# Performance work log

Measured on AMD Instinct MI355X. Metric: run time of the kernel, lower is better.

## Reference

```python
import jax, jax.numpy as jnp
import numpy as np

TOP_K = 2


def setup_inputs() -> dict:
    key = jax.random.key(0)
    k_x, k_g, k_w1, k_w2, k_w3 = jax.random.split(key, 5)
    B, S, D, H, E = 2, 512, 1024, 512, 8
    x = jax.random.normal(k_x, (B, S, D), dtype=jnp.float32)
    gate_w = jax.random.normal(k_g, (D, E), dtype=jnp.float32) * (D ** -0.5)
    w1 = jax.random.normal(k_w1, (E, D, H), dtype=jnp.float32) * 0.02  # gate proj
    w2 = jax.random.normal(k_w2, (E, H, D), dtype=jnp.float32) * 0.02  # down proj
    w3 = jax.random.normal(k_w3, (E, D, H), dtype=jnp.float32) * 0.02  # up proj
    return {"x": x, "gate_w": gate_w, "w1": w1, "w2": w2, "w3": w3}


def reference(x, gate_w, w1, w2, w3):
    # Token-choice top-k MoE with grouped SwiGLU experts, no shared expert.
    # Equivalent to torchtune MoE: gather routed tokens, scale by top-k router
    # score, run per-expert FFN, scatter-add back. Since each expert's FFN has
    # no bias (FFN(0) == 0), the dispatch/grouped-GEMM/combine is expressed
    # densely as sum_e FFN_e(scale[:, e] * x), which is mathematically identical.
    B, S, D = x.shape
    E = gate_w.shape[1]
    xf = x.reshape(B * S, D)                      # [T, D]
    T = B * S

    logits = xf @ gate_w                          # [T, E]
    scores = jax.nn.softmax(logits, axis=-1)
    top_scores, top_idx = jax.lax.top_k(scores, TOP_K)  # [T, k]

    # scale[t, e] = router score if expert e selected for token t, else 0
    scale = jnp.zeros((T, E), dtype=x.dtype).at[
        jnp.arange(T)[:, None], top_idx
    ].set(top_scores)

    xs = scale.T[:, :, None] * xf[None, :, :]     # [E, T, D] scaled routed input
    h = jax.nn.silu(jnp.einsum('etd,edh->eth', xs, w1)) \
        * jnp.einsum('etd,edh->eth', xs, w3)      # [E, T, H]
    y = jnp.einsum('eth,ehd->etd', h, w2)         # [E, T, D]
    out = y.sum(axis=0)                           # combine (scatter-add equiv)
    return out.reshape(B, S, D)
```

## Files before the change

kernel.cpp:

```cpp
#include <hip/hip_runtime.h>
#include <hip/hip_bf16.h>
#include <cstddef>

#define T_TOK 1024
#define D_DIM 1024
#define H_DIM 512
#define E_EXP 8
#define P_CAP 2560
#define MAX_MT (P_CAP / 64)
#define LDA 72

typedef __attribute__((ext_vector_type(4))) float    float4_t;
typedef __attribute__((ext_vector_type(8))) short    short8_t;
typedef __attribute__((ext_vector_type(4))) unsigned uint4_t;

__device__ __forceinline__ short f2bf(float f) {
  union { float f; unsigned u; } v; v.f = f;
  unsigned u = v.u;
  u += 0x7FFFu + ((u >> 16) & 1u);
  return (short)(u >> 16);
}

__device__ __forceinline__ unsigned pkbf(float a, float b) {
  union { __hip_bfloat162 h; unsigned u; } v;
  v.h = __float22bfloat162_rn(make_float2(a, b));
  return v.u;
}

__global__ __launch_bounds__(256) void prep_kernel(
    const float* __restrict__ w1, const float* __restrict__ w3,
    const float* __restrict__ w2, const float* __restrict__ x,
    const float* __restrict__ gw, short* __restrict__ w13t,
    short* __restrict__ w2t, int* __restrict__ idx2,
    float* __restrict__ scale2, float* __restrict__ out) {
  __shared__ float tile[64][68];
  const int z = blockIdx.z;
  const int tid = threadIdx.x;

  if (z < 24) {
    const float* src; short* dst; int N, ldd, row_off;
    if (z < 16) {
      if (blockIdx.y >= 8) return;
      int which = z >> 3, e = z & 7;
      src = (which ? w3 : w1) + (size_t)e * D_DIM * H_DIM;
      dst = w13t + (size_t)e * D_DIM * (2 * H_DIM);
      N = H_DIM; ldd = D_DIM; row_off = which ? H_DIM : 0;
    } else {
      if (blockIdx.x >= 8) return;
      int e = z - 16;
      src = w2 + (size_t)e * H_DIM * D_DIM;
      dst = w2t + (size_t)e * D_DIM * H_DIM;
      N = D_DIM; ldd = H_DIM; row_off = 0;
    }
    const int k0 = blockIdx.x * 64, n0 = blockIdx.y * 64;
    const int kr = tid >> 4, nc = (tid & 15) * 4;
    #pragma unroll
    for (int p = 0; p < 4; ++p) {
      int k = p * 16 + kr;
      float4_t v = *(const float4_t*)(src + (size_t)(k0 + k) * N + n0 + nc);
      *(float4_t*)&tile[k][nc] = v;
    }
    __syncthreads();
    const int r8 = tid >> 3, c8 = tid & 7;
    #pragma unroll
    for (int p = 0; p < 2; ++p) {
      int row = p * 32 + r8;
      uint4_t u;
      #pragma unroll
      for (int j = 0; j < 4; ++j)
        u[j] = pkbf(tile[c8 * 8 + 2 * j][row], tile[c8 * 8 + 2 * j + 1][row]);
      *(uint4_t*)(dst + (size_t)(row_off + n0 + row) * ldd + k0 + c8 * 8) = u;
    }
    return;
  }

  if (z == 25) {
    float4_t z4 = {0.f, 0.f, 0.f, 0.f};
    float4_t* o = (float4_t*)(out + ((size_t)(blockIdx.y * 16 + blockIdx.x)) * 4096);
    #pragma unroll
    for (int i = 0; i < 4; ++i) o[i * 256 + tid] = z4;
    return;
  }

  const int wid  = tid >> 6;
  const int lane = tid & 63;
  const int t = (blockIdx.y * 16 + blockIdx.x) * 4 + wid;
  const float* xr = x + (size_t)t * D_DIM;
  float acc[E_EXP];
  #pragma unroll
  for (int e = 0; e < E_EXP; ++e) acc[e] = 0.f;
  for (int d = lane; d < D_DIM; d += 64) {
    float xv = xr[d];
    float4_t g0 = *(const float4_t*)(gw + d * E_EXP);
    float4_t g1 = *(const float4_t*)(gw + d * E_EXP + 4);
    acc[0] += xv * g0[0]; acc[1] += xv * g0[1];
    acc[2] += xv * g0[2]; acc[3] += xv * g0[3];
    acc[4] += xv * g1[0]; acc[5] += xv * g1[1];
    acc[6] += xv * g1[2]; acc[7] += xv * g1[3];
  }
  #pragma unroll
  for (int off = 32; off >= 1; off >>= 1) {
    #pragma unroll
    for (int e = 0; e < E_EXP; ++e) acc[e] += __shfl_down(acc[e], off, 64);
  }
  if (lane == 0) {
    float m = acc[0];
    #pragma unroll
    for (int e = 1; e < E_EXP; ++e) m = fmaxf(m, acc[e]);
    float p[E_EXP]; float s = 0.f;
    #pragma unroll
    for (int e = 0; e < E_EXP; ++e) { p[e] = __expf(acc[e] - m); s += p[e]; }
    float inv = 1.f / s;
    #pragma unroll
    for (int e = 0; e < E_EXP; ++e) p[e] *= inv;
    int i1 = 0;
    #pragma unroll
    for (int e = 1; e < E_EXP; ++e) if (p[e] > p[i1]) i1 = e;
    int i2 = (i1 == 0) ? 1 : 0;
    #pragma unroll
    for (int e = 0; e < E_EXP; ++e) {
      if (e == i1 || e == i2) continue;
      if (p[e] > p[i2]) i2 = e;
    }
    idx2[2 * t]     = i1;  scale2[2 * t]     = p[i1];
    idx2[2 * t + 1] = i2;  scale2[2 * t + 1] = p[i2];
  }
}

__global__ __launch_bounds__(256) void scan_kernel(
    const int* __restrict__ idx2, const float* __restrict__ scale2,
    int* __restrict__ pair_tok, float* __restrict__ pair_scale,
    int* __restrict__ meta) {
  __shared__ int cnt[E_EXP], base[E_EXP], cur[E_EXP];
  const int tid = threadIdx.x;
  if (tid < E_EXP) { cnt[tid] = 0; cur[tid] = 0; }
  for (int p = tid; p < P_CAP; p += 256) { pair_tok[p] = -1; pair_scale[p] = 0.f; }
  __syncthreads();
  for (int t = tid; t < T_TOK; t += 256) {
    atomicAdd(&cnt[idx2[2 * t]], 1);
    atomicAdd(&cnt[idx2[2 * t + 1]], 1);
  }
  __syncthreads();
  if (tid == 0) {
    int b = 0, g = 0;
    for (int e = 0; e < E_EXP; ++e) {
      base[e] = b;
      int al = (cnt[e] + 63) & ~63;
      for (int j = 0; j < al; j += 64) { meta[1 + g] = e; meta[41 + g] = b + j; ++g; }
      b += al;
    }
    meta[0] = g;
  }
  __syncthreads();
  for (int t = tid; t < T_TOK; t += 256) {
    #pragma unroll
    for (int s = 0; s < 2; ++s) {
      int e = idx2[2 * t + s];
      int p = base[e] + atomicAdd(&cur[e], 1);
      pair_tok[p] = t;
      pair_scale[p] = scale2[2 * t + s];
    }
  }
}

__global__ __launch_bounds__(256, 4) void gemm1_kernel(
    const float* __restrict__ x, const short* __restrict__ w13t,
    const int* __restrict__ pair_tok, const float* __restrict__ pair_scale,
    const int* __restrict__ meta, short* __restrict__ h) {
  __shared__ short As[64 * LDA];
  __shared__ short B1s[32 * LDA];
  __shared__ short B3s[32 * LDA];
  const int mt = blockIdx.y;
  if (mt >= meta[0]) return;
  const int e    = meta[1 + mt];
  const int row0 = meta[41 + mt];
  const int n0   = blockIdx.x * 32;
  const int tid = threadIdx.x, lane = tid & 63, wid = tid >> 6;
  const int wr = wid >> 1, wc = wid & 1;
  const int q = lane >> 4, ln = lane & 15;
  const short* bsrc = w13t + (size_t)e * D_DIM * (2 * H_DIM);

  const int ar = tid >> 2, ak = (tid & 3) * 16;
  const int   tokr = pair_tok[row0 + ar];
  const float sc   = pair_scale[row0 + ar];
  const float* xrow = x + (size_t)(tokr < 0 ? 0 : tokr) * D_DIM + ak;
  const int br = tid >> 3, bu = (tid & 7) * 8;
  const short* b1p = bsrc + (size_t)(n0 + br) * D_DIM + bu;
  const short* b3p = bsrc + (size_t)(H_DIM + n0 + br) * D_DIM + bu;

  float4_t acc1[2], acc3[2];
  acc1[0] = acc1[1] = acc3[0] = acc3[1] = (float4_t){0.f, 0.f, 0.f, 0.f};

  for (int k0 = 0; k0 < D_DIM; k0 += 64) {
    float4_t v0 = *(const float4_t*)(xrow + k0);
    float4_t v1 = *(const float4_t*)(xrow + k0 + 4);
    float4_t v2 = *(const float4_t*)(xrow + k0 + 8);
    float4_t v3 = *(const float4_t*)(xrow + k0 + 12);
    uint4_t vb1 = *(const uint4_t*)(b1p + k0);
    uint4_t vb3 = *(const uint4_t*)(b3p + k0);
    uint4_t u0 = {pkbf(v0[0] * sc, v0[1] * sc), pkbf(v0[2] * sc, v0[3] * sc),
                  pkbf(v1[0] * sc, v1[1] * sc), pkbf(v1[2] * sc, v1[3] * sc)};
    uint4_t u1 = {pkbf(v2[0] * sc, v2[1] * sc), pkbf(v2[2] * sc, v2[3] * sc),
                  pkbf(v3[0] * sc, v3[1] * sc), pkbf(v3[2] * sc, v3[3] * sc)};
    *(uint4_t*)&As[ar * LDA + ak]     = u0;
    *(uint4_t*)&As[ar * LDA + ak + 8] = u1;
    *(uint4_t*)&B1s[br * LDA + bu] = vb1;
    *(uint4_t*)&B3s[br * LDA + bu] = vb3;
    __syncthreads();

    short8_t af[2][2], b1f[2], b3f[2];
    #pragma unroll
    for (int i = 0; i < 2; ++i)
      #pragma unroll
      for (int kk = 0; kk < 2; ++kk)
        af[i][kk] = *(const short8_t*)&As[(wr * 32 + i * 16 + ln) * LDA + kk * 32 + q * 8];
    #pragma unroll
    for (int kk = 0; kk < 2; ++kk) {
      b1f[kk] = *(const short8_t*)&B1s[(wc * 16 + ln) * LDA + kk * 32 + q * 8];
      b3f[kk] = *(const short8_t*)&B3s[(wc * 16 + ln) * LDA + kk * 32 + q * 8];
    }
    #pragma unroll
    for (int i = 0; i < 2; ++i)
      #pragma unroll
      for (int kk = 0; kk < 2; ++kk) {
        acc1[i] = __builtin_amdgcn_mfma_f32_16x16x32_bf16(af[i][kk], b1f[kk], acc1[i], 0, 0, 0);
        acc3[i] = __builtin_amdgcn_mfma_f32_16x16x32_bf16(af[i][kk], b3f[kk], acc3[i], 0, 0, 0);
      }
    __syncthreads();
  }

  #pragma unroll
  for (int i = 0; i < 2; ++i) {
    int r_base = row0 + wr * 32 + i * 16 + q * 4;
    int col = n0 + wc * 16 + ln;
    #pragma unroll
    for (int rr = 0; rr < 4; ++rr) {
      float c1 = acc1[i][rr];
      float c3 = acc3[i][rr];
      float sig = 1.f / (1.f + __expf(-c1));
      h[(size_t)(r_base + rr) * H_DIM + col] = f2bf(c1 * sig * c3);
    }
  }
}

__global__ __launch_bounds__(256, 4) void gemm2_kernel(
    const short* __restrict__ h, const short* __restrict__ w2t,
    const int* __restrict__ pair_tok, const int* __restrict__ meta,
    float* __restrict__ out) {
  __shared__ short As[64 * LDA];
  __shared__ short Bs[64 * LDA];
  const int mt = blockIdx.y;
  if (mt >= meta[0]) return;
  const int e    = meta[1 + mt];
  const int row0 = meta[41 + mt];
  const int n0   = blockIdx.x * 64;
  const int tid = threadIdx.x, lane = tid & 63, wid = tid >> 6;
  const int wr = wid >> 1, wc = wid & 1;
  const int q = lane >> 4, ln = lane & 15;
  const short* bsrc = w2t + (size_t)e * D_DIM * H_DIM;

  const int ar = tid >> 2, ak = (tid & 3) * 16;
  const short* arow = h + (size_t)(row0 + ar) * H_DIM + ak;
  const short* brow = bsrc + (size_t)(n0 + ar) * H_DIM + ak;

  float4_t acc[2][2];
  #pragma unroll
  for (int i = 0; i < 2; ++i)
    #pragma unroll
    for (int j = 0; j < 2; ++j) acc[i][j] = (float4_t){0.f, 0.f, 0.f, 0.f};

  for (int k0 = 0; k0 < H_DIM; k0 += 64) {
    uint4_t va0 = *(const uint4_t*)(arow + k0);
    uint4_t va1 = *(const uint4_t*)(arow + k0 + 8);
    uint4_t vb0 = *(const uint4_t*)(brow + k0);
    uint4_t vb1 = *(const uint4_t*)(brow + k0 + 8);
    *(uint4_t*)&As[ar * LDA + ak]     = va0;
    *(uint4_t*)&As[ar * LDA + ak + 8] = va1;
    *(uint4_t*)&Bs[ar * LDA + ak]     = vb0;
    *(uint4_t*)&Bs[ar * LDA + ak + 8] = vb1;
    __syncthreads();

    short8_t af[2][2], bf[2][2];
    #pragma unroll
    for (int i = 0; i < 2; ++i)
      #pragma unroll
      for (int kk = 0; kk < 2; ++kk) {
        af[i][kk] = *(const short8_t*)&As[(wr * 32 + i * 16 + ln) * LDA + kk * 32 + q * 8];
        bf[i][kk] = *(const short8_t*)&Bs[(wc * 32 + i * 16 + ln) * LDA + kk * 32 + q * 8];
      }
    #pragma unroll
    for (int i = 0; i < 2; ++i)
      #pragma unroll
      for (int j = 0; j < 2; ++j)
        #pragma unroll
        for (int kk = 0; kk < 2; ++kk)
          acc[i][j] = __builtin_amdgcn_mfma_f32_16x16x32_bf16(af[i][kk], bf[j][kk], acc[i][j], 0, 0, 0);
    __syncthreads();
  }

  #pragma unroll
  for (int i = 0; i < 2; ++i) {
    int r_base = row0 + wr * 32 + i * 16 + q * 4;
    #pragma unroll
    for (int rr = 0; rr < 4; ++rr) {
      int tok = pair_tok[r_base + rr];
      if (tok < 0) continue;
      float* orow = out + (size_t)tok * D_DIM;
      #pragma unroll
      for (int j = 0; j < 2; ++j) {
        int col = n0 + wc * 32 + j * 16 + ln;
        atomicAdd(orow + col, acc[i][j][rr]);
      }
    }
  }
}

extern "C" void kernel_launch(void* const* d_in, const int* in_sizes, int n_in,
                              void* d_out, int out_size, void* d_ws, size_t ws_size,
                              hipStream_t stream) {
  const float* x  = (const float*)d_in[0];
  const float* gw = (const float*)d_in[1];
  const float* w1 = (const float*)d_in[2];
  const float* w2 = (const float*)d_in[3];
  const float* w3 = (const float*)d_in[4];
  float* out = (float*)d_out;

  char* ws = (char*)d_ws;
  int*   idx2    = (int*)  (ws);
  float* scale2  = (float*)(ws + 8192);
  int*   ptok    = (int*)  (ws + 16384);
  float* pscale  = (float*)(ws + 32768);
  int*   meta    = (int*)  (ws + 49152);
  short* h       = (short*)(ws + (1u << 20));
  short* w13t    = (short*)(ws + (4u << 20));
  short* w2t     = (short*)(ws + (21u << 20));

  prep_kernel<<<dim3(16, 16, 26), dim3(256), 0, stream>>>(
      w1, w3, w2, x, gw, w13t, w2t, idx2, scale2, out);
  scan_kernel<<<dim3(1), dim3(256), 0, stream>>>(idx2, scale2, ptok, pscale, meta);
  gemm1_kernel<<<dim3(H_DIM / 32, MAX_MT), dim3(256), 0, stream>>>(
      x, w13t, ptok, pscale, meta, h);
  gemm2_kernel<<<dim3(D_DIM / 64, MAX_MT), dim3(256), 0, stream>>>(
      h, w2t, ptok, meta, out);
}
```

Measured before the change: 150.7 us.

## Fuse all four MoE stages into one cooperative persistent kernel with grid syncs

Replaces the four separate launches (prep, scan, gemm1, gemm2) with one cooperative kernel. A persistent grid loops over jobs for each phase, and grid.sync() separates the phases. The goal is to remove launch gaps and the idle tail of grids sized for the worst case, since the GEMM loops now run only over the real number of M-tiles. The cost is grid-wide barriers, a scan phase where only block 0 works while the rest of the grid waits, and lower occupancy from launch_bounds(256,2) and the shared smem buffer.

Measured after the change: 416.8 us. +176.5%, slower.

```diff
diff --git a/kernel.cpp b/kernel.cpp
--- a/kernel.cpp
+++ b/kernel.cpp
@@ -1,13 +1,15 @@
 #include <hip/hip_runtime.h>
+#include <hip/hip_cooperative_groups.h>
 #include <hip/hip_bf16.h>
 #include <cstddef>
+
+namespace cg = cooperative_groups;
 
 #define T_TOK 1024
 #define D_DIM 1024
 #define H_DIM 512
 #define E_EXP 8
 #define P_CAP 2560
-#define MAX_MT (P_CAP / 64)
 #define LDA 72
 
 typedef __attribute__((ext_vector_type(4))) float    float4_t;
@@ -27,289 +29,282 @@
   return v.u;
 }
 
-__global__ __launch_bounds__(256) void prep_kernel(
+__global__ __launch_bounds__(256, 2) void fused_kernel(
     const float* __restrict__ w1, const float* __restrict__ w3,
     const float* __restrict__ w2, const float* __restrict__ x,
     const float* __restrict__ gw, short* __restrict__ w13t,
     short* __restrict__ w2t, int* __restrict__ idx2,
-    float* __restrict__ scale2, float* __restrict__ out) {
-  __shared__ float tile[64][68];
-  const int z = blockIdx.z;
+    float* __restrict__ scale2, int* __restrict__ pair_tok,
+    float* __restrict__ pair_scale, int* __restrict__ meta,
+    short* __restrict__ h, float* __restrict__ out) {
+  cg::grid_group grid = cg::this_grid();
+  __shared__ __align__(16) char smem[18432];
+  const int bid = blockIdx.x;
+  const int nb  = gridDim.x;
   const int tid = threadIdx.x;
-
-  if (z < 24) {
-    const float* src; short* dst; int N, ldd, row_off;
-    if (z < 16) {
-      if (blockIdx.y >= 8) return;
-      int which = z >> 3, e = z & 7;
-      src = (which ? w3 : w1) + (size_t)e * D_DIM * H_DIM;
-      dst = w13t + (size_t)e * D_DIM * (2 * H_DIM);
-      N = H_DIM; ldd = D_DIM; row_off = which ? H_DIM : 0;
+  const int lane = tid & 63, wid = tid >> 6;
+
+  for (int j = bid; j < 3584; j += nb) {
+    if (j < 3072) {
+      float (*tile)[68] = (float(*)[68])smem;
+      int z = j >> 7, sub = j & 127;
+      const float* src; short* dst; int N, ldd, row_off, xt, yt;
+      if (z < 16) {
+        int which = z >> 3, e = z & 7;
+        src = (which ? w3 : w1) + (size_t)e * D_DIM * H_DIM;
+        dst = w13t + (size_t)e * D_DIM * (2 * H_DIM);
+        N = H_DIM; ldd = D_DIM; row_off = which ? H_DIM : 0;
+        xt = sub >> 3; yt = sub & 7;
+      } else {
+        int e = z - 16;
+        src = w2 + (size_t)e * H_DIM * D_DIM;
+        dst = w2t + (size_t)e * D_DIM * H_DIM;
+        N = D_DIM; ldd = H_DIM; row_off = 0;
+        xt = sub & 7; yt = sub >> 3;
+      }
+      const int k0 = xt * 64, n0 = yt * 64;
+      const int kr = tid >> 4, nc = (tid & 15) * 4;
+      #pragma unroll
+      for (int p = 0; p < 4; ++p) {
+        int k = p * 16 + kr;
+        float4_t v = *(const float4_t*)(src + (size_t)(k0 + k) * N + n0 + nc);
+        *(float4_t*)&tile[k][nc] = v;
+      }
+      __syncthreads();
+      const int r8 = tid >> 3, c8 = tid & 7;
+      #pragma unroll
+      for (int p = 0; p < 2; ++p) {
+        int row = p * 32 + r8;
+        uint4_t u;
+        #pragma unroll
+        for (int jj = 0; jj < 4; ++jj)
+          u[jj] = pkbf(tile[c8 * 8 + 2 * jj][row], tile[c8 * 8 + 2 * jj + 1][row]);
+        *(uint4_t*)(dst + (size_t)(row_off + n0 + row) * ldd + k0 + c8 * 8) = u;
+      }
+      __syncthreads();
+    } else if (j < 3328) {
+      const int t = (j - 3072) * 4 + wid;
+      const float* xr = x + (size_t)t * D_DIM;
+      float acc[E_EXP];
+      #pragma unroll
+      for (int e = 0; e < E_EXP; ++e) acc[e] = 0.f;
+      for (int d = lane; d < D_DIM; d += 64) {
+        float xv = xr[d];
+        float4_t g0 = *(const float4_t*)(gw + d * E_EXP);
+        float4_t g1 = *(const float4_t*)(gw + d * E_EXP + 4);
+        acc[0] += xv * g0[0]; acc[1] += xv * g0[1];
+        acc[2] += xv * g0[2]; acc[3] += xv * g0[3];
+        acc[4] += xv * g1[0]; acc[5] += xv * g1[1];
+        acc[6] += xv * g1[2]; acc[7] += xv * g1[3];
+      }
+      #pragma unroll
+      for (int off = 32; off >= 1; off >>= 1) {
+        #pragma unroll
+        for (int e = 0; e < E_EXP; ++e) acc[e] += __shfl_down(acc[e], off, 64);
+      }
+      if (lane == 0) {
+        float m = acc[0];
+        #pragma unroll
+        for (int e = 1; e < E_EXP; ++e) m = fmaxf(m, acc[e]);
+        float p[E_EXP]; float s = 0.f;
+        #pragma unroll
+        for (int e = 0; e < E_EXP; ++e) { p[e] = __expf(acc[e] - m); s += p[e]; }
+        float inv = 1.f / s;
+        #pragma unroll
+        for (int e = 0; e < E_EXP; ++e) p[e] *= inv;
+        int i1 = 0;
+        #pragma unroll
+        for (int e = 1; e < E_EXP; ++e) if (p[e] > p[i1]) i1 = e;
+        int i2 = (i1 == 0) ? 1 : 0;
+        #pragma unroll
+        for (int e = 0; e < E_EXP; ++e) {
+          if (e == i1 || e == i2) continue;
+          if (p[e] > p[i2]) i2 = e;
+        }
+        idx2[2 * t]     = i1;  scale2[2 * t]     = p[i1];
+        idx2[2 * t + 1] = i2;  scale2[2 * t + 1] = p[i2];
+      }
     } else {
-      if (blockIdx.x >= 8) return;
-      int e = z - 16;
-      src = w2 + (size_t)e * H_DIM * D_DIM;
-      dst = w2t + (size_t)e * D_DIM * H_DIM;
-      N = D_DIM; ldd = H_DIM; row_off = 0;
-    }
-    const int k0 = blockIdx.x * 64, n0 = blockIdx.y * 64;
-    const int kr = tid >> 4, nc = (tid & 15) * 4;
+      float4_t z4 = {0.f, 0.f, 0.f, 0.f};
+      float4_t* o = (float4_t*)(out + (size_t)(j - 3328) * 4096);
+      #pragma unroll
+      for (int i = 0; i < 4; ++i) o[i * 256 + tid] = z4;
+    }
+  }
+  grid.sync();
+
+  if (bid == 0) {
+    __shared__ int cnt[E_EXP], base[E_EXP], cur[E_EXP];
+    if (tid < E_EXP) { cnt[tid] = 0; cur[tid] = 0; }
+    for (int p = tid; p < P_CAP; p += 256) { pair_tok[p] = -1; pair_scale[p] = 0.f; }
+    __syncthreads();
+    for (int t = tid; t < T_TOK; t += 256) {
+      atomicAdd(&cnt[idx2[2 * t]], 1);
+      atomicAdd(&cnt[idx2[2 * t + 1]], 1);
+    }
+    __syncthreads();
+    if (tid == 0) {
+      int b = 0, g = 0;
+      for (int e = 0; e < E_EXP; ++e) {
+        base[e] = b;
+        int al = (cnt[e] + 63) & ~63;
+        for (int jj = 0; jj < al; jj += 64) { meta[1 + g] = e; meta[41 + g] = b + jj; ++g; }
+        b += al;
+      }
+      meta[0] = g;
+    }
+    __syncthreads();
+    for (int t = tid; t < T_TOK; t += 256) {
+      #pragma unroll
+      for (int s = 0; s < 2; ++s) {
+        int e = idx2[2 * t + s];
+        int p = base[e] + atomicAdd(&cur[e], 1);
+        pair_tok[p] = t;
+        pair_scale[p] = scale2[2 * t + s];
+      }
+    }
+  }
+  grid.sync();
+
+  const int n_mt = meta[0];
+  const int wr = (tid >> 6) >> 1, wc = (tid >> 6) & 1;
+  const int q = lane >> 4, ln = lane & 15;
+
+  for (int job = bid; job < 16 * n_mt; job += nb) {
+    short* As  = (short*)smem;
+    short* B1s = As + 64 * LDA;
+    short* B3s = B1s + 32 * LDA;
+    const int mt   = job >> 4;
+    const int e    = meta[1 + mt];
+    const int row0 = meta[41 + mt];
+    const int n0   = (job & 15) * 32;
+    const short* bsrc = w13t + (size_t)e * D_DIM * (2 * H_DIM);
+
+    const int ar = tid >> 2, ak = (tid & 3) * 16;
+    const int   tokr = pair_tok[row0 + ar];
+    const float sc   = pair_scale[row0 + ar];
+    const float* xrow = x + (size_t)(tokr < 0 ? 0 : tokr) * D_DIM + ak;
+    const int br = tid >> 3, bu = (tid & 7) * 8;
+    const short* b1p = bsrc + (size_t)(n0 + br) * D_DIM + bu;
+    const short* b3p = bsrc + (size_t)(H_DIM + n0 + br) * D_DIM + bu;
+
+    float4_t acc1[2], acc3[2];
+    acc1[0] = acc1[1] = acc3[0] = acc3[1] = (float4_t){0.f, 0.f, 0.f, 0.f};
+
+    for (int k0 = 0; k0 < D_DIM; k0 += 64) {
+      float4_t v0 = *(const float4_t*)(xrow + k0);
+      float4_t v1 = *(const float4_t*)(xrow + k0 + 4);
+      float4_t v2 = *(const float4_t*)(xrow + k0 + 8);
+      float4_t v3 = *(const float4_t*)(xrow + k0 + 12);
+      uint4_t vb1 = *(const uint4_t*)(b1p + k0);
+      uint4_t vb3 = *(const uint4_t*)(b3p + k0);
+      uint4_t u0 = {pkbf(v0[0] * sc, v0[1] * sc), pkbf(v0[2] * sc, v0[3] * sc),
+                    pkbf(v1[0] * sc, v1[1] * sc), pkbf(v1[2] * sc, v1[3] * sc)};
+      uint4_t u1 = {pkbf(v2[0] * sc, v2[1] * sc), pkbf(v2[2] * sc, v2[3] * sc),
+                    pkbf(v3[0] * sc, v3[1] * sc), pkbf(v3[2] * sc, v3[3] * sc)};
+      *(uint4_t*)&As[ar * LDA + ak]     = u0;
+      *(uint4_t*)&As[ar * LDA + ak + 8] = u1;
+      *(uint4_t*)&B1s[br * LDA + bu] = vb1;
+      *(uint4_t*)&B3s[br * LDA + bu] = vb3;
+      __syncthreads();
+
+      short8_t af[2][2], b1f[2], b3f[2];
+      #pragma unroll
+      for (int i = 0; i < 2; ++i)
+        #pragma unroll
+        for (int kk = 0; kk < 2; ++kk)
+          af[i][kk] = *(const short8_t*)&As[(wr * 32 + i * 16 + ln) * LDA + kk * 32 + q * 8];
+      #pragma unroll
+      for (int kk = 0; kk < 2; ++kk) {
+        b1f[kk] = *(const short8_t*)&B1s[(wc * 16 + ln) * LDA + kk * 32 + q * 8];
+        b3f[kk] = *(const short8_t*)&B3s[(wc * 16 + ln) * LDA + kk * 32 + q * 8];
+      }
+      #pragma unroll
+      for (int i = 0; i < 2; ++i)
+        #pragma unroll
+        for (int kk = 0; kk < 2; ++kk) {
+          acc1[i] = __builtin_amdgcn_mfma_f32_16x16x32_bf16(af[i][kk], b1f[kk], acc1[i], 0, 0, 0);
+          acc3[i] = __builtin_amdgcn_mfma_f32_16x16x32_bf16(af[i][kk], b3f[kk], acc3[i], 0, 0, 0);
+        }
+      __syncthreads();
+    }
+
     #pragma unroll
-    for (int p = 0; p < 4; ++p) {
-      int k = p * 16 + kr;
-      float4_t v = *(const float4_t*)(src + (size_t)(k0 + k) * N + n0 + nc);
-      *(float4_t*)&tile[k][nc] = v;
-    }
-    __syncthreads();
-    const int r8 = tid >> 3, c8 = tid & 7;
-    #pragma unroll
-    for (int p = 0; p < 2; ++p) {
-      int row = p * 32 + r8;
-      uint4_t u;
-      #pragma unroll
-      for (int j = 0; j < 4; ++j)
-        u[j] = pkbf(tile[c8 * 8 + 2 * j][row], tile[c8 * 8 + 2 * j + 1][row]);
-      *(uint4_t*)(dst + (size_t)(row_off + n0 + row) * ldd + k0 + c8 * 8) = u;
-    }
-    return;
+    for (int i = 0; i < 2; ++i) {
+      int r_base = row0 + wr * 32 + i * 16 + q * 4;
+      int col = n0 + wc * 16 + ln;
+      #pragma unroll
+      for (int rr = 0; rr < 4; ++rr) {
+        float c1 = acc1[i][rr];
+        float c3 = acc3[i][rr];
+        float sig = 1.f / (1.f + __expf(-c1));
+        h[(size_t)(r_base + rr) * H_DIM + col] = f2bf(c1 * sig * c3);
+      }
+    }
   }
-
-  if (z == 25) {
-    float4_t z4 = {0.f, 0.f, 0.f, 0.f};
-    float4_t* o = (float4_t*)(out + ((size_t)(blockIdx.y * 16 + blockIdx.x)) * 4096);
-    #pragma unroll
-    for (int i = 0; i < 4; ++i) o[i * 256 + tid] = z4;
-    return;
-  }
-
-  const int wid  = tid >> 6;
-  const int lane = tid & 63;
-  const int t = (blockIdx.y * 16 + blockIdx.x) * 4 + wid;
-  const float* xr = x + (size_t)t * D_DIM;
-  float acc[E_EXP];
-  #pragma unroll
-  for (int e = 0; e < E_EXP; ++e) acc[e] = 0.f;
-  for (int d = lane; d < D_DIM; d += 64) {
-    float xv = xr[d];
-    float4_t g0 = *(const float4_t*)(gw + d * E_EXP);
-    float4_t g1 = *(const float4_t*)(gw + d * E_EXP + 4);
-    acc[0] += xv * g0[0]; acc[1] += xv * g0[1];
-    acc[2] += xv * g0[2]; acc[3] += xv * g0[3];
-    acc[4] += xv * g1[0]; acc[5] += xv * g1[1];
-    acc[6] += xv * g1[2]; acc[7] += xv * g1[3];
-  }
-  #pragma unroll
-  for (int off = 32; off >= 1; off >>= 1) {
-    #pragma unroll
-    for (int e = 0; e < E_EXP; ++e) acc[e] += __shfl_down(acc[e], off, 64);
-  }
-  if (lane == 0) {
-    float m = acc[0];
-    #pragma unroll
-    for (int e = 1; e < E_EXP; ++e) m = fmaxf(m, acc[e]);
-    float p[E_EXP]; float s = 0.f;
-    #pragma unroll
-    for (int e = 0; e < E_EXP; ++e) { p[e] = __expf(acc[e] - m); s += p[e]; }
-    float inv = 1.f / s;
-    #pragma unroll
-    for (int e = 0; e < E_EXP; ++e) p[e] *= inv;
-    int i1 = 0;
-    #pragma unroll
-    for (int e = 1; e < E_EXP; ++e) if (p[e] > p[i1]) i1 = e;
-    int i2 = (i1 == 0) ? 1 : 0;
-    #pragma unroll
-    for (int e = 0; e < E_EXP; ++e) {
-      if (e == i1 || e == i2) continue;
-      if (p[e] > p[i2]) i2 = e;
-    }
-    idx2[2 * t]     = i1;  scale2[2 * t]     = p[i1];
-    idx2[2 * t + 1] = i2;  scale2[2 * t + 1] = p[i2];
-  }
-}
-
-__global__ __launch_bounds__(256) void scan_kernel(
-    const int* __restrict__ idx2, const float* __restrict__ scale2,
-    int* __restrict__ pair_tok, float* __restrict__ pair_scale,
-    int* __restrict__ meta) {
-  __shared__ int cnt[E_EXP], base[E_EXP], cur[E_EXP];
-  const int tid = threadIdx.x;
-  if (tid < E_EXP) { cnt[tid] = 0; cur[tid] = 0; }
-  for (int p = tid; p < P_CAP; p += 256) { pair_tok[p] = -1; pair_scale[p] = 0.f; }
-  __syncthreads();
-  for (int t = tid; t < T_TOK; t += 256) {
-    atomicAdd(&cnt[idx2[2 * t]], 1);
-    atomicAdd(&cnt[idx2[2 * t + 1]], 1);
-  }
-  __syncthreads();
-  if (tid == 0) {
-    int b = 0, g = 0;
-    for (int e = 0; e < E_EXP; ++e) {
-      base[e] = b;
-      int al = (cnt[e] + 63) & ~63;
-      for (int j = 0; j < al; j += 64) { meta[1 + g] = e; meta[41 + g] = b + j; ++g; }
-      b += al;
-    }
-    meta[0] = g;
-  }
-  __syncthreads();
-  for (int t = tid; t < T_TOK; t += 256) {
-    #pragma unroll
-    for (int s = 0; s < 2; ++s) {
-      int e = idx2[2 * t + s];
-      int p = base[e] + atomicAdd(&cur[e], 1);
-      pair_tok[p] = t;
-      pair_scale[p] = scale2[2 * t + s];
-    }
-  }
-}
-
-__global__ __launch_bounds__(256, 4) void gemm1_kernel(
-    const float* __restrict__ x, const short* __restrict__ w13t,
-    const int* __restrict__ pair_tok, const float* __restrict__ pair_scale,
-    const int* __restrict__ meta, short* __restrict__ h) {
-  __shared__ short As[64 * LDA];
-  __shared__ short B1s[32 * LDA];
-  __shared__ short B3s[32 * LDA];
-  const int mt = blockIdx.y;
-  if (mt >= meta[0]) return;
-  const int e    = meta[1 + mt];
-  const int row0 = meta[41 + mt];
-  const int n0   = blockIdx.x * 32;
-  const int tid = threadIdx.x, lane = tid & 63, wid = tid >> 6;
-  const int wr = wid >> 1, wc = wid & 1;
-  const int q = lane >> 4, ln = lane & 15;
-  const short* bsrc = w13t + (size_t)e * D_DIM * (2 * H_DIM);
-
-  const int ar = tid >> 2, ak = (tid & 3) * 16;
-  const int   tokr = pair_tok[row0 + ar];
-  const float sc   = pair_scale[row0 + ar];
-  const float* xrow = x + (size_t)(tokr < 0 ? 0 : tokr) * D_DIM + ak;
-  const int br = tid >> 3, bu = (tid & 7) * 8;
-  const short* b1p = bsrc + (size_t)(n0 + br) * D_DIM + bu;
-  const short* b3p = bsrc + (size_t)(H_DIM + n0 + br) * D_DIM + bu;
-
-  float4_t acc1[2], acc3[2];
-  acc1[0] = acc1[1] = acc3[0] = acc3[1] = (float4_t){0.f, 0.f, 0.f, 0.f};
-
-  for (int k0 = 0; k0 < D_DIM; k0 += 64) {
-    float4_t v0 = *(const float4_t*)(xrow + k0);
-    float4_t v1 = *(const float4_t*)(xrow + k0 + 4);
-    float4_t v2 = *(const float4_t*)(xrow + k0 + 8);
-    float4_t v3 = *(const float4_t*)(xrow + k0 + 12);
-    uint4_t vb1 = *(const uint4_t*)(b1p + k0);
-    uint4_t vb3 = *(const uint4_t*)(b3p + k0);
-    uint4_t u0 = {pkbf(v0[0] * sc, v0[1] * sc), pkbf(v0[2] * sc, v0[3] * sc),
-                  pkbf(v1[0] * sc, v1[1] * sc), pkbf(v1[2] * sc, v1[3] * sc)};
-    uint4_t u1 = {pkbf(v2[0] * sc, v2[1] * sc), pkbf(v2[2] * sc, v2[3] * sc),
-                  pkbf(v3[0] * sc, v3[1] * sc), pkbf(v3[2] * sc, v3[3] * sc)};
-    *(uint4_t*)&As[ar * LDA + ak]     = u0;
-    *(uint4_t*)&As[ar * LDA + ak + 8] = u1;
-    *(uint4_t*)&B1s[br * LDA + bu] = vb1;
-    *(uint4_t*)&B3s[br * LDA + bu] = vb3;
-    __syncthreads();
-
-    short8_t af[2][2], b1f[2], b3f[2];
+  grid.sync();
+
+  for (int job = bid; job < 16 * n_mt; job += nb) {
+    short* As = (short*)smem;
+    short* Bs = As + 64 * LDA;
+    const int mt   = job >> 4;
+    const int e    = meta[1 + mt];
+    const int row0 = meta[41 + mt];
+    const int n0   = (job & 15) * 64;
+    const short* bsrc = w2t + (size_t)e * D_DIM * H_DIM;
+
+    const int ar = tid >> 2, ak = (tid & 3) * 16;
+    const short* arow = h + (size_t)(row0 + ar) * H_DIM + ak;
+    const short* brow = bsrc + (size_t)(n0 + ar) * H_DIM + ak;
+
+    float4_t acc[2][2];
     #pragma unroll
     for (int i = 0; i < 2; ++i)
       #pragma unroll
-      for (int kk = 0; kk < 2; ++kk)
-        af[i][kk] = *(const short8_t*)&As[(wr * 32 + i * 16 + ln) * LDA + kk * 32 + q * 8];
+      for (int jj = 0; jj < 2; ++jj) acc[i][jj] = (float4_t){0.f, 0.f, 0.f, 0.f};
+
+    for (int k0 = 0; k0 < H_DIM; k0 += 64) {
+      uint4_t va0 = *(const uint4_t*)(arow + k0);
+      uint4_t va1 = *(const uint4_t*)(arow + k0 + 8);
+      uint4_t vb0 = *(const uint4_t*)(brow + k0);
+      uint4_t vb1 = *(const uint4_t*)(brow + k0 + 8);
+      *(uint4_t*)&As[ar * LDA + ak]     = va0;
+      *(uint4_t*)&As[ar * LDA + ak + 8] = va1;
+      *(uint4_t*)&Bs[ar * LDA + ak]     = vb0;
+      *(uint4_t*)&Bs[ar * LDA + ak + 8] = vb1;
+      __syncthreads();
+
+      short8_t af[2][2], bf[2][2];
+      #pragma unroll
+      for (int i = 0; i < 2; ++i)
+        #pragma unroll
+        for (int kk = 0; kk < 2; ++kk) {
+          af[i][kk] = *(const short8_t*)&As[(wr * 32 + i * 16 + ln) * LDA + kk * 32 + q * 8];
+          bf[i][kk] = *(const short8_t*)&Bs[(wc * 32 + i * 16 + ln) * LDA + kk * 32 + q * 8];
+        }
+      #pragma unroll
+      for (int i = 0; i < 2; ++i)
+        #pragma unroll
+        for (int jj = 0; jj < 2; ++jj)
+          #pragma unroll
+          for (int kk = 0; kk < 2; ++kk)
+            acc[i][jj] = __builtin_amdgcn_mfma_f32_16x16x32_bf16(af[i][kk], bf[jj][kk], acc[i][jj], 0, 0, 0);
+      __syncthreads();
+    }
+
     #pragma unroll
-    for (int kk = 0; kk < 2; ++kk) {
-      b1f[kk] = *(const short8_t*)&B1s[(wc * 16 + ln) * LDA + kk * 32 + q * 8];
-      b3f[kk] = *(const short8_t*)&B3s[(wc * 16 + ln) * LDA + kk * 32 + q * 8];
-    }
-    #pragma unroll
-    for (int i = 0; i < 2; ++i)
-      #pragma unroll
-      for (int kk = 0; kk < 2; ++kk) {
-        acc1[i] = __builtin_amdgcn_mfma_f32_16x16x32_bf16(af[i][kk], b1f[kk], acc1[i], 0, 0, 0);
-        acc3[i] = __builtin_amdgcn_mfma_f32_16x16x32_bf16(af[i][kk], b3f[kk], acc3[i], 0, 0, 0);
-      }
-    __syncthreads();
-  }
-
-  #pragma unroll
-  for (int i = 0; i < 2; ++i) {
-    int r_base = row0 + wr * 32 + i * 16 + q * 4;
-    int col = n0 + wc * 16 + ln;
-    #pragma unroll
-    for (int rr = 0; rr < 4; ++rr) {
-      float c1 = acc1[i][rr];
-      float c3 = acc3[i][rr];
-      float sig = 1.f / (1.f + __expf(-c1));
-      h[(size_t)(r_base + rr) * H_DIM + col] = f2bf(c1 * sig * c3);
-    }
-  }
-}
-
-__global__ __launch_bounds__(256, 4) void gemm2_kernel(
-    const short* __restrict__ h, const short* __restrict__ w2t,
-    const int* __restrict__ pair_tok, const int* __restrict__ meta,
-    float* __restrict__ out) {
-  __shared__ short As[64 * LDA];
-  __shared__ short Bs[64 * LDA];
-  const int mt = blockIdx.y;
-  if (mt >= meta[0]) return;
-  const int e    = meta[1 + mt];
-  const int row0 = meta[41 + mt];
-  const int n0   = blockIdx.x * 64;
-  const int tid = threadIdx.x, lane = tid & 63, wid = tid >> 6;
-  const int wr = wid >> 1, wc = wid & 1;
-  const int q = lane >> 4, ln = lane & 15;
-  const short* bsrc = w2t + (size_t)e * D_DIM * H_DIM;
-
-  const int ar = tid >> 2, ak = (tid & 3) * 16;
-  const short* arow = h + (size_t)(row0 + ar) * H_DIM + ak;
-  const short* brow = bsrc + (size_t)(n0 + ar) * H_DIM + ak;
-
-  float4_t acc[2][2];
-  #pragma unroll
-  for (int i = 0; i < 2; ++i)
-    #pragma unroll
-    for (int j = 0; j < 2; ++j) acc[i][j] = (float4_t){0.f, 0.f, 0.f, 0.f};
-
-  for (int k0 = 0; k0 < H_DIM; k0 += 64) {
-    uint4_t va0 = *(const uint4_t*)(arow + k0);
-    uint4_t va1 = *(const uint4_t*)(arow + k0 + 8);
-    uint4_t vb0 = *(const uint4_t*)(brow + k0);
-    uint4_t vb1 = *(const uint4_t*)(brow + k0 + 8);
-    *(uint4_t*)&As[ar * LDA + ak]     = va0;
-    *(uint4_t*)&As[ar * LDA + ak + 8] = va1;
-    *(uint4_t*)&Bs[ar * LDA + ak]     = vb0;
-    *(uint4_t*)&Bs[ar * LDA + ak + 8] = vb1;
-    __syncthreads();
-
-    short8_t af[2][2], bf[2][2];
-    #pragma unroll
-    for (int i = 0; i < 2; ++i)
-      #pragma unroll
-      for (int kk = 0; kk < 2; ++kk) {
-        af[i][kk] = *(const short8_t*)&As[(wr * 32 + i * 16 + ln) * LDA + kk * 32 + q * 8];
-        bf[i][kk] = *(const short8_t*)&Bs[(wc * 32 + i * 16 + ln) * LDA + kk * 32 + q * 8];
-      }
-    #pragma unroll
-    for (int i = 0; i < 2; ++i)
-      #pragma unroll
-      for (int j = 0; j < 2; ++j)
-        #pragma unroll
-        for (int kk = 0; kk < 2; ++kk)
-          acc[i][j] = __builtin_amdgcn_mfma_f32_16x16x32_bf16(af[i][kk], bf[j][kk], acc[i][j], 0, 0, 0);
-    __syncthreads();
-  }
-
-  #pragma unroll
-  for (int i = 0; i < 2; ++i) {
-    int r_base = row0 + wr * 32 + i * 16 + q * 4;
-    #pragma unroll
-    for (int rr = 0; rr < 4; ++rr) {
-      int tok = pair_tok[r_base + rr];
-      if (tok < 0) continue;
-      float* orow = out + (size_t)tok * D_DIM;
-      #pragma unroll
-      for (int j = 0; j < 2; ++j) {
-        int col = n0 + wc * 32 + j * 16 + ln;
-        atomicAdd(orow + col, acc[i][j][rr]);
+    for (int i = 0; i < 2; ++i) {
+      int r_base = row0 + wr * 32 + i * 16 + q * 4;
+      #pragma unroll
+      for (int rr = 0; rr < 4; ++rr) {
+        int tok = pair_tok[r_base + rr];
+        if (tok < 0) continue;
+        float* orow = out + (size_t)tok * D_DIM;
+        #pragma unroll
+        for (int jj = 0; jj < 2; ++jj) {
+          int col = n0 + wc * 32 + jj * 16 + ln;
+          atomicAdd(orow + col, acc[i][jj][rr]);
+        }
       }
     }
   }
@@ -321,8 +316,8 @@
   const float* x  = (const float*)d_in[0];
   const float* gw = (const float*)d_in[1];
   const float* w1 = (const float*)d_in[2];
+  const float* w3 = (const float*)d_in[4];
   const float* w2 = (const float*)d_in[3];
-  const float* w3 = (const float*)d_in[4];
   float* out = (float*)d_out;
 
   char* ws = (char*)d_ws;
@@ -335,11 +330,15 @@
   short* w13t    = (short*)(ws + (4u << 20));
   short* w2t     = (short*)(ws + (21u << 20));
 
-  prep_kernel<<<dim3(16, 16, 26), dim3(256), 0, stream>>>(
-      w1, w3, w2, x, gw, w13t, w2t, idx2, scale2, out);
-  scan_kernel<<<dim3(1), dim3(256), 0, stream>>>(idx2, scale2, ptok, pscale, meta);
-  gemm1_kernel<<<dim3(H_DIM / 32, MAX_MT), dim3(256), 0, stream>>>(
-      x, w13t, ptok, pscale, meta, h);
-  gemm2_kernel<<<dim3(D_DIM / 64, MAX_MT), dim3(256), 0, stream>>>(
-      h, w2t, ptok, meta, out);
+  int maxb = 0;
+  if (hipOccupancyMaxActiveBlocksPerMultiprocessor(
+          &maxb, (const void*)fused_kernel, 256, 0) != hipSuccess || maxb < 1)
+    maxb = 1;
+  int grid = maxb * 256;
+  if (grid > 1024) grid = 1024;
+
+  void* kargs[] = {&w1, &w3, &w2, &x, &gw, &w13t, &w2t, &idx2, &scale2,
+                   &ptok, &pscale, &meta, &h, &out};
+  hipLaunchCooperativeKernel((const void*)fused_kernel, dim3(grid), dim3(256),
+                             kargs, 0, stream);
 }
```

## Fuse routing scan into GEMM kernels and pad transpose tile to avoid bank conflicts

Applied to the files above, without the earlier changes.

Removes the single-block scan kernel launch. Each GEMM block now recomputes expert counts, a prefix sum and its own 64-row token/scale list in shared memory straight from idx2. This drops one serialized launch and the global pair_tok/pair_scale/meta buffers, at the cost of redundant scan work and extra barriers in every GEMM block. The prep transpose tile is also padded to 69 columns with scalar stores to reduce LDS bank conflicts on the column read.

Measured after the change: 165.9 us. +10.1%, slower.

```diff
diff --git a/kernel.cpp b/kernel.cpp
--- a/kernel.cpp
+++ b/kernel.cpp
@@ -6,8 +6,7 @@
 #define D_DIM 1024
 #define H_DIM 512
 #define E_EXP 8
-#define P_CAP 2560
-#define MAX_MT (P_CAP / 64)
+#define MAX_MT 40
 #define LDA 72
 
 typedef __attribute__((ext_vector_type(4))) float    float4_t;
@@ -33,7 +32,7 @@
     const float* __restrict__ gw, short* __restrict__ w13t,
     short* __restrict__ w2t, int* __restrict__ idx2,
     float* __restrict__ scale2, float* __restrict__ out) {
-  __shared__ float tile[64][68];
+  __shared__ float tile[64][69];
   const int z = blockIdx.z;
   const int tid = threadIdx.x;
 
@@ -58,7 +57,10 @@
     for (int p = 0; p < 4; ++p) {
       int k = p * 16 + kr;
       float4_t v = *(const float4_t*)(src + (size_t)(k0 + k) * N + n0 + nc);
-      *(float4_t*)&tile[k][nc] = v;
+      tile[k][nc]     = v[0];
+      tile[k][nc + 1] = v[1];
+      tile[k][nc + 2] = v[2];
+      tile[k][nc + 3] = v[3];
     }
     __syncthreads();
     const int r8 = tid >> 3, c8 = tid & 7;
@@ -67,8 +69,8 @@
       int row = p * 32 + r8;
       uint4_t u;
       #pragma unroll
-      for (int j = 0; j < 4; ++j)
-        u[j] = pkbf(tile[c8 * 8 + 2 * j][row], tile[c8 * 8 + 2 * j + 1][row]);
+      for (int jj = 0; jj < 4; ++jj)
+        u[jj] = pkbf(tile[c8 * 8 + 2 * jj][row], tile[c8 * 8 + 2 * jj + 1][row]);
       *(uint4_t*)(dst + (size_t)(row_off + n0 + row) * ldd + k0 + c8 * 8) = u;
     }
     return;
@@ -127,62 +129,98 @@
   }
 }
 
-__global__ __launch_bounds__(256) void scan_kernel(
-    const int* __restrict__ idx2, const float* __restrict__ scale2,
-    int* __restrict__ pair_tok, float* __restrict__ pair_scale,
-    int* __restrict__ meta) {
-  __shared__ int cnt[E_EXP], base[E_EXP], cur[E_EXP];
-  const int tid = threadIdx.x;
-  if (tid < E_EXP) { cnt[tid] = 0; cur[tid] = 0; }
-  for (int p = tid; p < P_CAP; p += 256) { pair_tok[p] = -1; pair_scale[p] = 0.f; }
+#define SCAN_DECLS                                                            \
+  __shared__ unsigned char sE[2048];                                          \
+  __shared__ unsigned char sLC[8 * 256];                                      \
+  __shared__ int scnt[8];                                                     \
+  __shared__ int spref[256];                                                  \
+  __shared__ int stok[64];                                                    \
+  __shared__ float ssc[64];
+
+#define SCAN_BODY(idx2_, scale2_, mt_, tid_, E_OUT, ROW0_OUT)                 \
+  {                                                                           \
+    uint4_t a4 = *(const uint4_t*)((idx2_) + (tid_) * 8);                     \
+    uint4_t b4 = *(const uint4_t*)((idx2_) + (tid_) * 8 + 4);                 \
+    unsigned char lc[8] = {0, 0, 0, 0, 0, 0, 0, 0};                           \
+    int ev[8] = {(int)a4[0], (int)a4[1], (int)a4[2], (int)a4[3],              \
+                 (int)b4[0], (int)b4[1], (int)b4[2], (int)b4[3]};             \
+    _Pragma("unroll")                                                         \
+    for (int i = 0; i < 8; ++i) {                                             \
+      int ee = ev[i]; lc[ee]++; sE[(tid_) * 8 + i] = (unsigned char)ee;       \
+    }                                                                         \
+    _Pragma("unroll")                                                         \
+    for (int ee = 0; ee < 8; ++ee) sLC[ee * 256 + (tid_)] = lc[ee];           \
+  }                                                                           \
+  __syncthreads();                                                            \
+  if ((tid_) < 8) {                                                           \
+    int s = 0; const unsigned char* pp = &sLC[(tid_) * 256];                  \
+    for (int j = 0; j < 256; ++j) s += pp[j];                                 \
+    scnt[(tid_)] = s;                                                         \
+  }                                                                           \
+  __syncthreads();                                                            \
+  int E_OUT = -1, ROW0_OUT = 0, mloc_ = 0, nmt_ = 0;                          \
+  {                                                                           \
+    int b = 0, ts = 0;                                                        \
+    _Pragma("unroll")                                                         \
+    for (int ee = 0; ee < 8; ++ee) {                                          \
+      int c = scnt[ee]; int nt = (c + 63) >> 6;                               \
+      if (E_OUT < 0 && (mt_) < ts + nt) {                                     \
+        E_OUT = ee; mloc_ = (mt_) - ts; ROW0_OUT = b + mloc_ * 64;            \
+      }                                                                       \
+      ts += nt; b += nt * 64;                                                 \
+    }                                                                         \
+    nmt_ = ts;                                                                \
+  }                                                                           \
+  if ((mt_) >= nmt_) return;                                                  \
+  const int cnt_e_ = scnt[E_OUT];                                             \
+  spref[(tid_)] = sLC[E_OUT * 256 + (tid_)];                                  \
+  __syncthreads();                                                            \
+  for (int off = 1; off < 256; off <<= 1) {                                   \
+    int v = ((tid_) >= off) ? spref[(tid_) - off] : 0;                        \
+    __syncthreads();                                                          \
+    spref[(tid_)] += v;                                                       \
+    __syncthreads();                                                          \
+  }                                                                           \
+  if ((tid_) < 64) {                                                          \
+    int R = mloc_ * 64 + (tid_);                                              \
+    int tok = -1; float sc = 0.f;                                             \
+    if (R < cnt_e_) {                                                         \
+      int c = 0;                                                              \
+      while (spref[c] <= R) ++c;                                              \
+      int need = R - (c ? spref[c - 1] : 0);                                  \
+      for (int i = 0; i < 8; ++i) {                                           \
+        if (sE[c * 8 + i] == (unsigned char)E_OUT) {                          \
+          if (need == 0) { int j = c * 8 + i; tok = j >> 1;                   \
+                           sc = (scale2_) ? (scale2_)[j] : 0.f; break; }      \
+          --need;                                                             \
+        }                                                                     \
+      }                                                                       \
+    }                                                                         \
+    stok[(tid_)] = tok; ssc[(tid_)] = sc;                                     \
+  }                                                                           \
   __syncthreads();
-  for (int t = tid; t < T_TOK; t += 256) {
-    atomicAdd(&cnt[idx2[2 * t]], 1);
-    atomicAdd(&cnt[idx2[2 * t + 1]], 1);
-  }
-  __syncthreads();
-  if (tid == 0) {
-    int b = 0, g = 0;
-    for (int e = 0; e < E_EXP; ++e) {
-      base[e] = b;
-      int al = (cnt[e] + 63) & ~63;
-      for (int j = 0; j < al; j += 64) { meta[1 + g] = e; meta[41 + g] = b + j; ++g; }
-      b += al;
-    }
-    meta[0] = g;
-  }
-  __syncthreads();
-  for (int t = tid; t < T_TOK; t += 256) {
-    #pragma unroll
-    for (int s = 0; s < 2; ++s) {
-      int e = idx2[2 * t + s];
-      int p = base[e] + atomicAdd(&cur[e], 1);
-      pair_tok[p] = t;
-      pair_scale[p] = scale2[2 * t + s];
-    }
-  }
-}
 
 __global__ __launch_bounds__(256, 4) void gemm1_kernel(
     const float* __restrict__ x, const short* __restrict__ w13t,
-    const int* __restrict__ pair_tok, const float* __restrict__ pair_scale,
-    const int* __restrict__ meta, short* __restrict__ h) {
+    const int* __restrict__ idx2, const float* __restrict__ scale2,
+    short* __restrict__ h) {
   __shared__ short As[64 * LDA];
   __shared__ short B1s[32 * LDA];
   __shared__ short B3s[32 * LDA];
-  const int mt = blockIdx.y;
-  if (mt >= meta[0]) return;
-  const int e    = meta[1 + mt];
-  const int row0 = meta[41 + mt];
+  SCAN_DECLS
+  const int mt  = blockIdx.y;
+  const int tid = threadIdx.x;
+  SCAN_BODY(idx2, scale2, mt, tid, e, row0)
+
   const int n0   = blockIdx.x * 32;
-  const int tid = threadIdx.x, lane = tid & 63, wid = tid >> 6;
+  const int lane = tid & 63, wid = tid >> 6;
   const int wr = wid >> 1, wc = wid & 1;
   const int q = lane >> 4, ln = lane & 15;
   const short* bsrc = w13t + (size_t)e * D_DIM * (2 * H_DIM);
 
   const int ar = tid >> 2, ak = (tid & 3) * 16;
-  const int   tokr = pair_tok[row0 + ar];
-  const float sc   = pair_scale[row0 + ar];
+  const int   tokr = stok[ar];
+  const float sc   = ssc[ar];
   const float* xrow = x + (size_t)(tokr < 0 ? 0 : tokr) * D_DIM + ak;
   const int br = tid >> 3, bu = (tid & 7) * 8;
   const short* b1p = bsrc + (size_t)(n0 + br) * D_DIM + bu;
@@ -245,16 +283,16 @@
 
 __global__ __launch_bounds__(256, 4) void gemm2_kernel(
     const short* __restrict__ h, const short* __restrict__ w2t,
-    const int* __restrict__ pair_tok, const int* __restrict__ meta,
-    float* __restrict__ out) {
+    const int* __restrict__ idx2, float* __restrict__ out) {
   __shared__ short As[64 * LDA];
   __shared__ short Bs[64 * LDA];
-  const int mt = blockIdx.y;
-  if (mt >= meta[0]) return;
-  const int e    = meta[1 + mt];
-  const int row0 = meta[41 + mt];
+  SCAN_DECLS
+  const int mt  = blockIdx.y;
+  const int tid = threadIdx.x;
+  SCAN_BODY(idx2, (const float*)nullptr, mt, tid, e, row0)
+
   const int n0   = blockIdx.x * 64;
-  const int tid = threadIdx.x, lane = tid & 63, wid = tid >> 6;
+  const int lane = tid & 63, wid = tid >> 6;
   const int wr = wid >> 1, wc = wid & 1;
   const int q = lane >> 4, ln = lane & 15;
   const short* bsrc = w2t + (size_t)e * D_DIM * H_DIM;
@@ -300,10 +338,10 @@
 
   #pragma unroll
   for (int i = 0; i < 2; ++i) {
-    int r_base = row0 + wr * 32 + i * 16 + q * 4;
+    int r_local = wr * 32 + i * 16 + q * 4;
     #pragma unroll
     for (int rr = 0; rr < 4; ++rr) {
-      int tok = pair_tok[r_base + rr];
+      int tok = stok[r_local + rr];
       if (tok < 0) continue;
       float* orow = out + (size_t)tok * D_DIM;
       #pragma unroll
@@ -328,18 +366,14 @@
   char* ws = (char*)d_ws;
   int*   idx2    = (int*)  (ws);
   float* scale2  = (float*)(ws + 8192);
-  int*   ptok    = (int*)  (ws + 16384);
-  float* pscale  = (float*)(ws + 32768);
-  int*   meta    = (int*)  (ws + 49152);
   short* h       = (short*)(ws + (1u << 20));
   short* w13t    = (short*)(ws + (4u << 20));
   short* w2t     = (short*)(ws + (21u << 20));
 
   prep_kernel<<<dim3(16, 16, 26), dim3(256), 0, stream>>>(
       w1, w3, w2, x, gw, w13t, w2t, idx2, scale2, out);
-  scan_kernel<<<dim3(1), dim3(256), 0, stream>>>(idx2, scale2, ptok, pscale, meta);
   gemm1_kernel<<<dim3(H_DIM / 32, MAX_MT), dim3(256), 0, stream>>>(
-      x, w13t, ptok, pscale, meta, h);
+      x, w13t, idx2, scale2, h);
   gemm2_kernel<<<dim3(D_DIM / 64, MAX_MT), dim3(256), 0, stream>>>(
-      h, w2t, ptok, meta, out);
-}
+      h, w2t, idx2, out);
+}
```
